# Performance work log

Measured on AMD Instinct MI355X. Metric: run time of the kernel, lower is better.

The kernel has to match this reference:

```python
import jax, jax.numpy as jnp
import numpy as np

D_MODEL = 1024
NUM_HEADS = 16
HEAD = D_MODEL // NUM_HEADS
SCALE = float(np.sqrt(D_MODEL))  # note: sqrt(d_model), as in source
LN_EPS = 1e-5


def setup_inputs() -> dict:
    key = jax.random.key(0)
    ks = jax.random.split(key, 12)
    B, Sq, Skv = 2, 2048, 2048
    s = 0.02
    return {
        "x": jax.random.normal(ks[0], (B, Sq, D_MODEL), jnp.float32),
        "enc_output": jax.random.normal(ks[1], (B, Skv, D_MODEL), jnp.float32),
        "Wq": jax.random.normal(ks[2], (D_MODEL, D_MODEL), jnp.float32) * s,
        "bq": jnp.zeros((D_MODEL,), jnp.float32),
        "Wk": jax.random.normal(ks[3], (D_MODEL, D_MODEL), jnp.float32) * s,
        "bk": jnp.zeros((D_MODEL,), jnp.float32),
        "Wv": jax.random.normal(ks[4], (D_MODEL, D_MODEL), jnp.float32) * s,
        "bv": jnp.zeros((D_MODEL,), jnp.float32),
        "Wo": jax.random.normal(ks[5], (D_MODEL, D_MODEL), jnp.float32) * s,
        "bo": jnp.zeros((D_MODEL,), jnp.float32),
        "gamma": jnp.ones((D_MODEL,), jnp.float32),
        "beta": jnp.zeros((D_MODEL,), jnp.float32),
    }


def _split_heads(t):
    B, S, _ = t.shape
    return t.reshape(B, S, NUM_HEADS, HEAD).transpose(0, 2, 1, 3)  # [B,H,S,hd]


def reference(x, enc_output, Wq, bq, Wk, bk, Wv, bv, Wo, bo, gamma, beta):
    q = _split_heads(x @ Wq.T + bq)           # [B,H,Sq,hd]
    k = _split_heads(enc_output @ Wk.T + bk)  # [B,H,Skv,hd]
    v = _split_heads(enc_output @ Wv.T + bv)  # [B,H,Skv,hd]
    scores = jnp.einsum("bhqd,bhkd->bhqk", q, k) / SCALE
    attn_weights = jax.nn.softmax(scores, axis=-1)  # dropout p=0 -> identity
    ctx = jnp.einsum("bhqk,bhkd->bhqd", attn_weights, v)
    B, H, Sq, hd = ctx.shape
    ctx = ctx.transpose(0, 2, 1, 3).reshape(B, Sq, H * hd)
    proj = ctx @ Wo.T + bo
    y = x + proj
    mu = jnp.mean(y, axis=-1, keepdims=True)
    var = jnp.var(y, axis=-1, keepdims=True)
    out = (y - mu) * jax.lax.rsqrt(var + LN_EPS) * gamma + beta
    return out, attn_weights
```

## Files before the change

### kernel.cpp

```cpp
#include <hip/hip_runtime.h>

typedef __attribute__((ext_vector_type(4))) float f32x4;
typedef __attribute__((ext_vector_type(8))) short bf16x8;
typedef __attribute__((ext_vector_type(4))) short s16x4;
typedef __attribute__((ext_vector_type(4))) unsigned u32x4;
typedef unsigned short u16;

#define GLOAD_LDS16(g, l)                                                      \
  __builtin_amdgcn_global_load_lds(                                            \
      (__attribute__((address_space(1))) const void*)(g),                      \
      (__attribute__((address_space(3))) void*)(l), 16, 0, 0)

static __device__ __forceinline__ u16 f2b(float f) {
  unsigned u = __builtin_bit_cast(unsigned, f);
  unsigned r = (u + 0x7fffu + ((u >> 16) & 1u)) >> 16;
  return (u16)r;
}

static __device__ __forceinline__ unsigned pk2(float lo, float hi) {
  unsigned r;
  asm("v_cvt_pk_bf16_f32 %0, %1, %2" : "=v"(r) : "v"(lo), "v"(hi));
  return r;
}

static __device__ __forceinline__ f32x4 mfma16(bf16x8 a, bf16x8 b, f32x4 c) {
  return __builtin_amdgcn_mfma_f32_16x16x32_bf16(a, b, c, 0, 0, 0);
}

static __device__ __forceinline__ int fsw(int row) {
  return (row & 7) ^ ((row & 8) >> 1);
}

__global__ __launch_bounds__(256) void cvt_bf16(const float* __restrict__ in,
                                                u16* __restrict__ out, int n4) {
  int i = blockIdx.x * 256 + threadIdx.x;
  int stride = gridDim.x * 256;
  for (; i < n4; i += stride) {
    float4 v = ((const float4*)in)[i];
    s16x4 o;
    o[0] = (short)f2b(v.x);
    o[1] = (short)f2b(v.y);
    o[2] = (short)f2b(v.z);
    o[3] = (short)f2b(v.w);
    ((s16x4*)out)[i] = o;
  }
}

__global__ __launch_bounds__(256) void cvt_w4(const float* __restrict__ w0,
                                              const float* __restrict__ w1,
                                              const float* __restrict__ w2,
                                              const float* __restrict__ w3,
                                              u16* __restrict__ o0,
                                              u16* __restrict__ o1,
                                              u16* __restrict__ o2,
                                              u16* __restrict__ o3) {
  int y = blockIdx.y;
  const float* in = (y == 0) ? w0 : (y == 1) ? w1 : (y == 2) ? w2 : w3;
  u16* out = (y == 0) ? o0 : (y == 1) ? o1 : (y == 2) ? o2 : o3;
  const int n4 = 262144;
  int i = blockIdx.x * 256 + threadIdx.x;
  int stride = gridDim.x * 256;
  for (; i < n4; i += stride) {
    float4 v = ((const float4*)in)[i];
    s16x4 o;
    o[0] = (short)f2b(v.x);
    o[1] = (short)f2b(v.y);
    o[2] = (short)f2b(v.z);
    o[3] = (short)f2b(v.w);
    ((s16x4*)out)[i] = o;
  }
}

#define QSCALE 0.0450842200278f
__global__ __launch_bounds__(256) void gemm_qkv3(
    const u16* __restrict__ xb, const u16* __restrict__ eb,
    const u16* __restrict__ Wqb, const u16* __restrict__ Wkb,
    const u16* __restrict__ Wvb, const float* __restrict__ bq,
    const float* __restrict__ bk, const float* __restrict__ bv,
    u16* __restrict__ Qd, u16* __restrict__ Kd, u16* __restrict__ Vtd) {
  __shared__ __align__(16) u16 As[128 * 32];
  __shared__ __align__(16) u16 Bs[128 * 32];
  const int K = 1024;
  int z = blockIdx.z;
  const u16* A = (z == 0) ? xb : eb;
  const u16* W = (z == 0) ? Wqb : (z == 1) ? Wkb : Wvb;
  const float* bias = (z == 0) ? bq : (z == 1) ? bk : bv;

  int tid = threadIdx.x;
  int w = tid >> 6, lane = tid & 63;
  int wr = w >> 1, wc = w & 1;
  int r16 = lane & 15, c4 = lane >> 4;
  int m0 = blockIdx.y * 128, n0 = blockIdx.x * 128;
  int srow = tid >> 2;
  int scol = (tid & 3) * 8;

  f32x4 acc[4][4] = {};

  const u16* ga0 = A + (size_t)(m0 + srow) * K + scol;
  const u16* gb0 = W + (size_t)(n0 + srow) * K + scol;
  char* asb = (char*)As + w * 1024;
  char* bsb = (char*)Bs + w * 1024;

  for (int k0 = 0; k0 < K; k0 += 32) {
    GLOAD_LDS16(ga0 + k0, asb);
    GLOAD_LDS16(ga0 + 64 * K + k0, asb + 4096);
    GLOAD_LDS16(gb0 + k0, bsb);
    GLOAD_LDS16(gb0 + 64 * K + k0, bsb + 4096);
    __syncthreads();
    bf16x8 af[4], bfr[4];
#pragma unroll
    for (int i = 0; i < 4; ++i)
      af[i] = *(const bf16x8*)(As + (wr * 64 + i * 16 + r16) * 32 + c4 * 8);
#pragma unroll
    for (int j = 0; j < 4; ++j)
      bfr[j] = *(const bf16x8*)(Bs + (wc * 64 + j * 16 + r16) * 32 + c4 * 8);
#pragma unroll
    for (int i = 0; i < 4; ++i)
#pragma unroll
      for (int j = 0; j < 4; ++j) acc[i][j] = mfma16(af[i], bfr[j], acc[i][j]);
    __syncthreads();
  }

  if (z < 2) {
    float oscale = (z == 0) ? QSCALE : 1.0f;
    u16* dst = (z == 0) ? Qd : Kd;
#pragma unroll
    for (int i = 0; i < 4; ++i) {
      int m = m0 + wr * 64 + i * 16 + c4 * 4;
      int b = m >> 11, s = m & 2047;
#pragma unroll
      for (int j = 0; j < 4; ++j) {
        int n = n0 + wc * 64 + j * 16 + r16;
        int h = n >> 6, d = n & 63;
        float bv = bias[n];
        u16* dp = dst + (((size_t)(b * 16 + h) * 2048 + s) * 64 + d);
#pragma unroll
        for (int r = 0; r < 4; ++r)
          dp[(size_t)r * 64] = f2b((acc[i][j][r] + bv) * oscale);
      }
    }
  } else {
#pragma unroll
    for (int i = 0; i < 4; ++i) {
      int m = m0 + wr * 64 + i * 16 + c4 * 4;
      int b = m >> 11, s = m & 2047;
#pragma unroll
      for (int j = 0; j < 4; ++j) {
        int n = n0 + wc * 64 + j * 16 + r16;
        int h = n >> 6, d = n & 63;
        float bv = bias[n];
        s16x4 o4;
#pragma unroll
        for (int r = 0; r < 4; ++r) o4[r] = (short)f2b(acc[i][j][r] + bv);
        *(s16x4*)(Vtd + ((size_t)((b * 16 + h) * 64 + d)) * 2048 + s) = o4;
      }
    }
  }
}

__global__ __launch_bounds__(256) void gemm_out(const u16* __restrict__ A,
                                                const u16* __restrict__ W,
                                                const float* __restrict__ bias,
                                                const float* __restrict__ X,
                                                float* __restrict__ Y) {
  __shared__ __align__(16) u16 As[128 * 32];
  __shared__ __align__(16) u16 Bs[128 * 32];
  const int K = 1024;
  int tid = threadIdx.x;
  int w = tid >> 6, lane = tid & 63;
  int wr = w >> 1, wc = w & 1;
  int r16 = lane & 15, c4 = lane >> 4;
  int m0 = blockIdx.y * 128, n0 = blockIdx.x * 128;
  int srow = tid >> 2;
  int scol = (tid & 3) * 8;

  f32x4 acc[4][4] = {};

  const u16* ga0 = A + (size_t)(m0 + srow) * K + scol;
  const u16* gb0 = W + (size_t)(n0 + srow) * K + scol;
  char* asb = (char*)As + w * 1024;
  char* bsb = (char*)Bs + w * 1024;

  for (int k0 = 0; k0 < K; k0 += 32) {
    GLOAD_LDS16(ga0 + k0, asb);
    GLOAD_LDS16(ga0 + 64 * K + k0, asb + 4096);
    GLOAD_LDS16(gb0 + k0, bsb);
    GLOAD_LDS16(gb0 + 64 * K + k0, bsb + 4096);
    __syncthreads();
    bf16x8 af[4], bfr[4];
#pragma unroll
    for (int i = 0; i < 4; ++i)
      af[i] = *(const bf16x8*)(As + (wr * 64 + i * 16 + r16) * 32 + c4 * 8);
#pragma unroll
    for (int j = 0; j < 4; ++j)
      bfr[j] = *(const bf16x8*)(Bs + (wc * 64 + j * 16 + r16) * 32 + c4 * 8);
#pragma unroll
    for (int i = 0; i < 4; ++i)
#pragma unroll
      for (int j = 0; j < 4; ++j) acc[i][j] = mfma16(af[i], bfr[j], acc[i][j]);
    __syncthreads();
  }

#pragma unroll
  for (int i = 0; i < 4; ++i) {
    int m = m0 + wr * 64 + i * 16 + c4 * 4;
#pragma unroll
    for (int j = 0; j < 4; ++j) {
      int n = n0 + wc * 64 + j * 16 + r16;
      float bv = bias[n];
#pragma unroll
      for (int r = 0; r < 4; ++r) {
        size_t idx = (size_t)(m + r) * 1024 + n;
        Y[idx] = acc[i][j][r] + bv + X[idx];
      }
    }
  }
}

__global__ __launch_bounds__(256, 4) void attn_k(const u16* __restrict__ Q,
                                                 const u16* __restrict__ Kg,
                                                 const u16* __restrict__ Vt,
                                                 float* __restrict__ attnw,
                                                 u16* __restrict__ ctx) {
  __shared__ __align__(16) u16 Klds[2][64 * 64];
  __shared__ __align__(16) u16 Vlds[2][64 * 64];

  int tid = threadIdx.x;
  int w = tid >> 6, lane = tid & 63;
  int r16 = lane & 15, c4 = lane >> 4;
  int id = blockIdx.x;
  int bh = id & 31, qt = id >> 5;
  int b = bh >> 4, h = bh & 15;
  int q0 = qt * 64 + w * 16;

  const u16* Qp = Q + ((size_t)bh * 2048 + q0) * 64;
  const u16* Kp = Kg + (size_t)bh * 2048 * 64;
  const u16* Vp = Vt + (size_t)bh * 64 * 2048;

  bf16x8 qf0 = *(const bf16x8*)(Qp + (size_t)r16 * 64 + c4 * 8);
  bf16x8 qf1 = *(const bf16x8*)(Qp + (size_t)r16 * 64 + 32 + c4 * 8);

  int perm0 = ((r16 >> 2) << 3) + (r16 & 3);
  int srow0 = w * 8 + (lane >> 3);
  int sc = lane & 7;

#define STAGE_K(bufi, kv)                                                      \
  {                                                                            \
    _Pragma("unroll") for (int i = 0; i < 2; ++i) {                            \
      int row = i * 32 + srow0;                                                \
      int ch = sc ^ fsw(row);                                                  \
      GLOAD_LDS16(Kp + (size_t)((kv) + row) * 64 + ch * 8,                     \
                  (u16*)&Klds[bufi][0] + w * 512 + i * 2048);                  \
    }                                                                          \
  }
#define STAGE_V(bufi, kv)                                                      \
  {                                                                            \
    _Pragma("unroll") for (int i = 0; i < 2; ++i) {                            \
      int row = i * 32 + srow0;                                                \
      int ch = sc ^ fsw(row);                                                  \
      GLOAD_LDS16(Vp + (size_t)row * 2048 + (kv) + ch * 8,                     \
                  (u16*)&Vlds[bufi][0] + w * 512 + i * 2048);                  \
    }                                                                          \
  }
#define LDSF(base, row, chunk)                                                 \
  (*(const bf16x8*)((base) + (row) * 64 + (((chunk) ^ fsw(row)) << 3)))
#define WAIT_BAR(n)                                                            \
  {                                                                            \
    asm volatile("s_waitcnt vmcnt(" #n ")" ::: "memory");                      \
    __builtin_amdgcn_s_barrier();                                              \
  }

  float sum = 0.f;
  STAGE_K(0, 0);
  WAIT_BAR(0);
  int buf = 0;
  for (int kv0 = 0; kv0 < 2048; kv0 += 64) {
    if (kv0 + 64 < 2048) STAGE_K(buf ^ 1, kv0 + 64);
    const u16* Kb = &Klds[buf][0];
#pragma unroll
    for (int s = 0; s < 2; ++s) {
      int ra = s * 32 + perm0;
      bf16x8 k00 = LDSF(Kb, ra, c4);
      bf16x8 k01 = LDSF(Kb, ra, c4 + 4);
      bf16x8 k10 = LDSF(Kb, ra + 4, c4);
      bf16x8 k11 = LDSF(Kb, ra + 4, c4 + 4);
      f32x4 s0 = {}, s1 = {};
      __builtin_amdgcn_s_setprio(1);
      s0 = mfma16(k00, qf0, s0);
      s0 = mfma16(k01, qf1, s0);
      s1 = mfma16(k10, qf0, s1);
      s1 = mfma16(k11, qf1, s1);
      __builtin_amdgcn_s_setprio(0);
#pragma unroll
      for (int r = 0; r < 4; ++r)
        sum += __builtin_amdgcn_exp2f(s0[r]) + __builtin_amdgcn_exp2f(s1[r]);
    }
    WAIT_BAR(2);
    buf ^= 1;
  }
  sum += __shfl_xor(sum, 16, 64);
  sum += __shfl_xor(sum, 32, 64);
  float nls = -__log2f(sum);

  f32x4 o[4] = {};
  float* ap = attnw + ((size_t)bh * 2048 + q0 + r16) * 2048;
  STAGE_K(0, 0);
  STAGE_V(0, 0);
  WAIT_BAR(0);
  buf = 0;
  for (int kv0 = 0; kv0 < 2048; kv0 += 64) {
    if (kv0 + 64 < 2048) {
      STAGE_K(buf ^ 1, kv0 + 64);
      STAGE_V(buf ^ 1, kv0 + 64);
    }
    const u16* Kb = &Klds[buf][0];
    const u16* Vb = &Vlds[buf][0];
#pragma unroll
    for (int s = 0; s < 2; ++s) {
      int ra = s * 32 + perm0;
      bf16x8 k00 = LDSF(Kb, ra, c4);
      bf16x8 k01 = LDSF(Kb, ra, c4 + 4);
      bf16x8 k10 = LDSF(Kb, ra + 4, c4);
      bf16x8 k11 = LDSF(Kb, ra + 4, c4 + 4);
      f32x4 s0 = {}, s1 = {};
      __builtin_amdgcn_s_setprio(1);
      s0 = mfma16(k00, qf0, s0);
      s0 = mfma16(k01, qf1, s0);
      s1 = mfma16(k10, qf0, s1);
      s1 = mfma16(k11, qf1, s1);
      __builtin_amdgcn_s_setprio(0);
      f32x4 p0, p1;
#pragma unroll
      for (int r = 0; r < 4; ++r) {
        p0[r] = __builtin_amdgcn_exp2f(s0[r] + nls);
        p1[r] = __builtin_amdgcn_exp2f(s1[r] + nls);
      }
      u32x4 pk;
      pk[0] = pk2(p0[0], p0[1]);
      pk[1] = pk2(p0[2], p0[3]);
      pk[2] = pk2(p1[0], p1[1]);
      pk[3] = pk2(p1[2], p1[3]);
      bf16x8 pf = __builtin_bit_cast(bf16x8, pk);
      bf16x8 v0 = LDSF(Vb, 0 * 16 + r16, s * 4 + c4);
      bf16x8 v1 = LDSF(Vb, 1 * 16 + r16, s * 4 + c4);
      bf16x8 v2 = LDSF(Vb, 2 * 16 + r16, s * 4 + c4);
      bf16x8 v3 = LDSF(Vb, 3 * 16 + r16, s * 4 + c4);
      __builtin_amdgcn_s_setprio(1);
      o[0] = mfma16(pf, v0, o[0]);
      o[1] = mfma16(pf, v1, o[1]);
      o[2] = mfma16(pf, v2, o[2]);
      o[3] = mfma16(pf, v3, o[3]);
      __builtin_amdgcn_s_setprio(0);
      int kvc = kv0 + s * 32 + c4 * 8;
      *(f32x4*)(ap + kvc) = p0;
      *(f32x4*)(ap + kvc + 4) = p1;
    }
    WAIT_BAR(4);
    buf ^= 1;
  }

#pragma unroll
  for (int dt = 0; dt < 4; ++dt)
#pragma unroll
    for (int r = 0; r < 4; ++r)
      ctx[((size_t)(b * 2048 + q0 + c4 * 4 + r)) * 1024 + h * 64 + dt * 16 +
          r16] = f2b(o[dt][r]);
#undef STAGE_K
#undef STAGE_V
#undef LDSF
#undef WAIT_BAR
}

__global__ __launch_bounds__(256) void ln_k(const float* __restrict__ Y,
                                            const float* __restrict__ gamma,
                                            const float* __restrict__ beta,
                                            float* __restrict__ out) {
  int row = blockIdx.x * 4 + (threadIdx.x >> 6);
  int lane = threadIdx.x & 63;
  const float* yr = Y + (size_t)row * 1024;
  float4 v[4];
  float sum = 0.f, sq = 0.f;
#pragma unroll
  for (int i = 0; i < 4; ++i) {
    v[i] = *(const float4*)(yr + i * 256 + lane * 4);
    sum += v[i].x + v[i].y + v[i].z + v[i].w;
    sq += v[i].x * v[i].x + v[i].y * v[i].y + v[i].z * v[i].z + v[i].w * v[i].w;
  }
#pragma unroll
  for (int m = 1; m < 64; m <<= 1) {
    sum += __shfl_xor(sum, m, 64);
    sq += __shfl_xor(sq, m, 64);
  }
  float mu = sum * (1.f / 1024.f);
  float var = sq * (1.f / 1024.f) - mu * mu;
  float rs = rsqrtf(var + 1e-5f);
  float* orow = out + (size_t)row * 1024;
#pragma unroll
  for (int i = 0; i < 4; ++i) {
    int c = i * 256 + lane * 4;
    float4 g = *(const float4*)(gamma + c);
    float4 be = *(const float4*)(beta + c);
    float4 o;
    o.x = (v[i].x - mu) * rs * g.x + be.x;
    o.y = (v[i].y - mu) * rs * g.y + be.y;
    o.z = (v[i].z - mu) * rs * g.z + be.z;
    o.w = (v[i].w - mu) * rs * g.w + be.w;
    *(float4*)(orow + c) = o;
  }
}

extern "C" void kernel_launch(void* const* d_in, const int* in_sizes, int n_in,
                              void* d_out, int out_size, void* d_ws,
                              size_t ws_size, hipStream_t stream) {
  const float* x = (const float*)d_in[0];
  const float* enc = (const float*)d_in[1];
  const float* Wq = (const float*)d_in[2];
  const float* bq = (const float*)d_in[3];
  const float* Wk = (const float*)d_in[4];
  const float* bk = (const float*)d_in[5];
  const float* Wv = (const float*)d_in[6];
  const float* bv = (const float*)d_in[7];
  const float* Wo = (const float*)d_in[8];
  const float* bo = (const float*)d_in[9];
  const float* gamma = (const float*)d_in[10];
  const float* beta = (const float*)d_in[11];

  float* out = (float*)d_out;
  float* attnw = out + (size_t)4194304;

  char* ws = (char*)d_ws;
  u16* xb = (u16*)(ws + (size_t)0);
  u16* eb = (u16*)(ws + ((size_t)8 << 20));
  u16* Wqb = (u16*)(ws + ((size_t)16 << 20));
  u16* Wkb = (u16*)(ws + ((size_t)18 << 20));
  u16* Wvb = (u16*)(ws + ((size_t)20 << 20));
  u16* Wob = (u16*)(ws + ((size_t)22 << 20));
  u16* Qws = (u16*)(ws + ((size_t)24 << 20));
  u16* Kws = (u16*)(ws + ((size_t)32 << 20));
  u16* Vt = (u16*)(ws + ((size_t)48 << 20));
  u16* ctx = (u16*)(ws + ((size_t)40 << 20));
  float* Yws = (float*)(ws + (size_t)0);

  cvt_bf16<<<dim3(1024), 256, 0, stream>>>(x, xb, 1048576);
  cvt_bf16<<<dim3(1024), 256, 0, stream>>>(enc, eb, 1048576);
  cvt_w4<<<dim3(256, 4), 256, 0, stream>>>(Wq, Wk, Wv, Wo, Wqb, Wkb, Wvb, Wob);

  gemm_qkv3<<<dim3(8, 32, 3), 256, 0, stream>>>(xb, eb, Wqb, Wkb, Wvb, bq, bk,
                                                bv, Qws, Kws, Vt);

  attn_k<<<dim3(1024), 256, 0, stream>>>(Qws, Kws, Vt, attnw, ctx);

  gemm_out<<<dim3(8, 32), 256, 0, stream>>>(ctx, Wob, bo, x, Yws);

  ln_k<<<dim3(1024), 256, 0, stream>>>(Yws, gamma, beta, out);
}
```

Measured before the change: 293.8 us.

## Triple-buffer K tiles in attention kernel to deepen prefetch pipeline

Moves K staging from two LDS buffers to three, so K loads run two tiles ahead in both the softmax-sum pass and the output pass. V stays double-buffered and is prefetched one tile ahead. Loads past the end wrap around with a mask instead of being guarded by a branch, and the vmcnt wait counts are adjusted to match. The aim is to hide global-to-LDS latency better, at the cost of more LDS per block (which may cut occupancy), redundant wraparound loads, and more outstanding memory operations.

Measured after the change: 298.2 us. Within noise of the previous version (+1.5%).

```diff
diff --git a/kernel.cpp b/kernel.cpp
--- a/kernel.cpp
+++ b/kernel.cpp
@@ -222,7 +222,7 @@
                                                  const u16* __restrict__ Vt,
                                                  float* __restrict__ attnw,
                                                  u16* __restrict__ ctx) {
-  __shared__ __align__(16) u16 Klds[2][64 * 64];
+  __shared__ __align__(16) u16 Klds[3][64 * 64];
   __shared__ __align__(16) u16 Vlds[2][64 * 64];
 
   int tid = threadIdx.x;
@@ -249,7 +249,7 @@
     _Pragma("unroll") for (int i = 0; i < 2; ++i) {                            \
       int row = i * 32 + srow0;                                                \
       int ch = sc ^ fsw(row);                                                  \
-      GLOAD_LDS16(Kp + (size_t)((kv) + row) * 64 + ch * 8,                     \
+      GLOAD_LDS16(Kp + (size_t)(((kv) & 2047) + row) * 64 + ch * 8,            \
                   (u16*)&Klds[bufi][0] + w * 512 + i * 2048);                  \
     }                                                                          \
   }
@@ -258,7 +258,7 @@
     _Pragma("unroll") for (int i = 0; i < 2; ++i) {                            \
       int row = i * 32 + srow0;                                                \
       int ch = sc ^ fsw(row);                                                  \
-      GLOAD_LDS16(Vp + (size_t)row * 2048 + (kv) + ch * 8,                     \
+      GLOAD_LDS16(Vp + (size_t)row * 2048 + ((kv) & 2047) + ch * 8,            \
                   (u16*)&Vlds[bufi][0] + w * 512 + i * 2048);                  \
     }                                                                          \
   }
@@ -272,31 +272,37 @@
 
   float sum = 0.f;
   STAGE_K(0, 0);
-  WAIT_BAR(0);
-  int buf = 0;
-  for (int kv0 = 0; kv0 < 2048; kv0 += 64) {
-    if (kv0 + 64 < 2048) STAGE_K(buf ^ 1, kv0 + 64);
-    const u16* Kb = &Klds[buf][0];
-#pragma unroll
-    for (int s = 0; s < 2; ++s) {
-      int ra = s * 32 + perm0;
-      bf16x8 k00 = LDSF(Kb, ra, c4);
-      bf16x8 k01 = LDSF(Kb, ra, c4 + 4);
-      bf16x8 k10 = LDSF(Kb, ra + 4, c4);
-      bf16x8 k11 = LDSF(Kb, ra + 4, c4 + 4);
-      f32x4 s0 = {}, s1 = {};
-      __builtin_amdgcn_s_setprio(1);
-      s0 = mfma16(k00, qf0, s0);
-      s0 = mfma16(k01, qf1, s0);
-      s1 = mfma16(k10, qf0, s1);
-      s1 = mfma16(k11, qf1, s1);
-      __builtin_amdgcn_s_setprio(0);
-#pragma unroll
-      for (int r = 0; r < 4; ++r)
-        sum += __builtin_amdgcn_exp2f(s0[r]) + __builtin_amdgcn_exp2f(s1[r]);
+  STAGE_K(1, 64);
+  WAIT_BAR(2);
+  {
+    int t = 0;
+    for (int kv0 = 0; kv0 < 2048; kv0 += 64, ++t) {
+      int b2 = t + 2;
+      b2 -= (b2 >= 3) ? 3 : 0;
+      STAGE_K(b2, kv0 + 128);
+      int bc = t;
+      bc -= (bc >= 3) ? ((bc >= 6) ? 6 : 3) : 0;
+      const u16* Kb = &Klds[bc % 3][0];
+#pragma unroll
+      for (int s = 0; s < 2; ++s) {
+        int ra = s * 32 + perm0;
+        bf16x8 k00 = LDSF(Kb, ra, c4);
+        bf16x8 k01 = LDSF(Kb, ra, c4 + 4);
+        bf16x8 k10 = LDSF(Kb, ra + 4, c4);
+        bf16x8 k11 = LDSF(Kb, ra + 4, c4 + 4);
+        f32x4 s0 = {}, s1 = {};
+        __builtin_amdgcn_s_setprio(1);
+        s0 = mfma16(k00, qf0, s0);
+        s0 = mfma16(k01, qf1, s0);
+        s1 = mfma16(k10, qf0, s1);
+        s1 = mfma16(k11, qf1, s1);
+        __builtin_amdgcn_s_setprio(0);
+#pragma unroll
+        for (int r = 0; r < 4; ++r)
+          sum += __builtin_amdgcn_exp2f(s0[r]) + __builtin_amdgcn_exp2f(s1[r]);
+      }
+      WAIT_BAR(2);
     }
-    WAIT_BAR(2);
-    buf ^= 1;
   }
   sum += __shfl_xor(sum, 16, 64);
   sum += __shfl_xor(sum, 32, 64);
@@ -304,59 +310,63 @@
 
   f32x4 o[4] = {};
   float* ap = attnw + ((size_t)bh * 2048 + q0 + r16) * 2048;
+  STAGE_V(0, 0);
   STAGE_K(0, 0);
-  STAGE_V(0, 0);
-  WAIT_BAR(0);
-  buf = 0;
-  for (int kv0 = 0; kv0 < 2048; kv0 += 64) {
-    if (kv0 + 64 < 2048) {
-      STAGE_K(buf ^ 1, kv0 + 64);
-      STAGE_V(buf ^ 1, kv0 + 64);
+  STAGE_K(1, 64);
+  WAIT_BAR(2);
+  {
+    int t = 0;
+    for (int kv0 = 0; kv0 < 2048; kv0 += 64, ++t) {
+      STAGE_V((t + 1) & 1, kv0 + 64);
+      int b2 = t + 2;
+      b2 -= (b2 >= 3) ? 3 : 0;
+      b2 -= (b2 >= 3) ? 3 : 0;
+      STAGE_K(b2, kv0 + 128);
+      int bc = t % 3;
+      const u16* Kb = &Klds[bc][0];
+      const u16* Vb = &Vlds[t & 1][0];
+#pragma unroll
+      for (int s = 0; s < 2; ++s) {
+        int ra = s * 32 + perm0;
+        bf16x8 k00 = LDSF(Kb, ra, c4);
+        bf16x8 k01 = LDSF(Kb, ra, c4 + 4);
+        bf16x8 k10 = LDSF(Kb, ra + 4, c4);
+        bf16x8 k11 = LDSF(Kb, ra + 4, c4 + 4);
+        f32x4 s0 = {}, s1 = {};
+        __builtin_amdgcn_s_setprio(1);
+        s0 = mfma16(k00, qf0, s0);
+        s0 = mfma16(k01, qf1, s0);
+        s1 = mfma16(k10, qf0, s1);
+        s1 = mfma16(k11, qf1, s1);
+        __builtin_amdgcn_s_setprio(0);
+        f32x4 p0, p1;
+#pragma unroll
+        for (int r = 0; r < 4; ++r) {
+          p0[r] = __builtin_amdgcn_exp2f(s0[r] + nls);
+          p1[r] = __builtin_amdgcn_exp2f(s1[r] + nls);
+        }
+        u32x4 pk;
+        pk[0] = pk2(p0[0], p0[1]);
+        pk[1] = pk2(p0[2], p0[3]);
+        pk[2] = pk2(p1[0], p1[1]);
+        pk[3] = pk2(p1[2], p1[3]);
+        bf16x8 pf = __builtin_bit_cast(bf16x8, pk);
+        bf16x8 v0 = LDSF(Vb, 0 * 16 + r16, s * 4 + c4);
+        bf16x8 v1 = LDSF(Vb, 1 * 16 + r16, s * 4 + c4);
+        bf16x8 v2 = LDSF(Vb, 2 * 16 + r16, s * 4 + c4);
+        bf16x8 v3 = LDSF(Vb, 3 * 16 + r16, s * 4 + c4);
+        __builtin_amdgcn_s_setprio(1);
+        o[0] = mfma16(pf, v0, o[0]);
+        o[1] = mfma16(pf, v1, o[1]);
+        o[2] = mfma16(pf, v2, o[2]);
+        o[3] = mfma16(pf, v3, o[3]);
+        __builtin_amdgcn_s_setprio(0);
+        int kvc = kv0 + s * 32 + c4 * 8;
+        *(f32x4*)(ap + kvc) = p0;
+        *(f32x4*)(ap + kvc + 4) = p1;
+      }
+      WAIT_BAR(6);
     }
-    const u16* Kb = &Klds[buf][0];
-    const u16* Vb = &Vlds[buf][0];
-#pragma unroll
-    for (int s = 0; s < 2; ++s) {
-      int ra = s * 32 + perm0;
-      bf16x8 k00 = LDSF(Kb, ra, c4);
-      bf16x8 k01 = LDSF(Kb, ra, c4 + 4);
-      bf16x8 k10 = LDSF(Kb, ra + 4, c4);
-      bf16x8 k11 = LDSF(Kb, ra + 4, c4 + 4);
-      f32x4 s0 = {}, s1 = {};
-      __builtin_amdgcn_s_setprio(1);
-      s0 = mfma16(k00, qf0, s0);
-      s0 = mfma16(k01, qf1, s0);
-      s1 = mfma16(k10, qf0, s1);
-      s1 = mfma16(k11, qf1, s1);
-      __builtin_amdgcn_s_setprio(0);
-      f32x4 p0, p1;
-#pragma unroll
-      for (int r = 0; r < 4; ++r) {
-        p0[r] = __builtin_amdgcn_exp2f(s0[r] + nls);
-        p1[r] = __builtin_amdgcn_exp2f(s1[r] + nls);
-      }
-      u32x4 pk;
-      pk[0] = pk2(p0[0], p0[1]);
-      pk[1] = pk2(p0[2], p0[3]);
-      pk[2] = pk2(p1[0], p1[1]);
-      pk[3] = pk2(p1[2], p1[3]);
-      bf16x8 pf = __builtin_bit_cast(bf16x8, pk);
-      bf16x8 v0 = LDSF(Vb, 0 * 16 + r16, s * 4 + c4);
-      bf16x8 v1 = LDSF(Vb, 1 * 16 + r16, s * 4 + c4);
-      bf16x8 v2 = LDSF(Vb, 2 * 16 + r16, s * 4 + c4);
-      bf16x8 v3 = LDSF(Vb, 3 * 16 + r16, s * 4 + c4);
-      __builtin_amdgcn_s_setprio(1);
-      o[0] = mfma16(pf, v0, o[0]);
-      o[1] = mfma16(pf, v1, o[1]);
-      o[2] = mfma16(pf, v2, o[2]);
-      o[3] = mfma16(pf, v3, o[3]);
-      __builtin_amdgcn_s_setprio(0);
-      int kvc = kv0 + s * 32 + c4 * 8;
-      *(f32x4*)(ap + kvc) = p0;
-      *(f32x4*)(ap + kvc + 4) = p1;
-    }
-    WAIT_BAR(4);
-    buf ^= 1;
   }
 
 #pragma unroll
```
